# Optimization experiments

Measured on AMD Instinct MI355X. Metric: run time of the kernel, lower is better.

## Reference

```python
import jax, jax.numpy as jnp
import numpy as np

KH = KW = 3
STRIDE = 1
PAD = 1
DIL = 1


def _bilinear_sample(x, py, px):
    """Zero-padded bilinear sampling.
    x: [B, C, H, W]; py, px: [B, K2, Ho, Wo] float sample coords.
    returns [B, C, K2, Ho, Wo].
    """
    B, C, H, W = x.shape
    y0 = jnp.floor(py)
    x0 = jnp.floor(px)
    wy1 = py - y0
    wx1 = px - x0
    wy0 = 1.0 - wy1
    wx0 = 1.0 - wx1
    xf = x.reshape(B, C, H * W)

    def gather(iy, ix):
        valid = (iy >= 0) & (iy <= H - 1) & (ix >= 0) & (ix <= W - 1)
        iyc = jnp.clip(iy, 0, H - 1).astype(jnp.int32)
        ixc = jnp.clip(ix, 0, W - 1).astype(jnp.int32)
        idx = (iyc * W + ixc).reshape(B, 1, -1)  # [B,1,K2*Ho*Wo]
        v = jnp.take_along_axis(xf, idx, axis=2)
        v = v.reshape(B, C, *iy.shape[1:])
        return v * valid[:, None].astype(x.dtype)

    return (gather(y0, x0) * (wy0 * wx0)[:, None]
            + gather(y0, x0 + 1) * (wy0 * wx1)[:, None]
            + gather(y0 + 1, x0) * (wy1 * wx0)[:, None]
            + gather(y0 + 1, x0 + 1) * (wy1 * wx1)[:, None])


def setup_inputs() -> dict:
    key = jax.random.key(0)
    k1, k2, k3, k4 = jax.random.split(key, 4)
    B, C, H, W = 8, 64, 128, 128
    Cout = 64
    K2 = KH * KW
    x = jax.random.normal(k1, (B, C, H, W), dtype=jnp.float32)
    offset = jax.random.normal(k2, (B, 2 * K2, H, W), dtype=jnp.float32)
    mask = jax.random.uniform(k3, (B, K2, H, W), dtype=jnp.float32)
    n = C * KH * KW
    stdv = 1.0 / np.sqrt(n)
    weight = jax.random.uniform(k4, (Cout, C, KH, KW), dtype=jnp.float32,
                                minval=-stdv, maxval=stdv)
    bias = jnp.zeros((Cout,), dtype=jnp.float32)
    return {"x": x, "offset": offset, "mask": mask, "weight": weight, "bias": bias}


def reference(x, offset, mask, weight, bias):
    B, C, H, W = x.shape
    Cout, Cin, kh, kw = weight.shape
    K2 = kh * kw
    Ho = (H + 2 * PAD - (DIL * (kh - 1) + 1)) // STRIDE + 1
    Wo = (W + 2 * PAD - (DIL * (kw - 1) + 1)) // STRIDE + 1
    # offset channels come interleaved per kernel location: ::2 -> x, 1::2 -> y
    off = offset.reshape(B, K2, 2, Ho, Wo)
    dx = off[:, :, 0]  # [B,K2,Ho,Wo]
    dy = off[:, :, 1]
    base_y = (STRIDE * jnp.arange(Ho) - PAD).astype(x.dtype)  # [Ho]
    base_x = (STRIDE * jnp.arange(Wo) - PAD).astype(x.dtype)  # [Wo]
    ky = (DIL * jnp.arange(kh)).astype(x.dtype)
    kx = (DIL * jnp.arange(kw)).astype(x.dtype)
    koff_y = jnp.repeat(ky, kw)  # [K2]
    koff_x = jnp.tile(kx, kh)    # [K2]
    py = base_y[None, None, :, None] + koff_y[None, :, None, None] + dy
    px = base_x[None, None, None, :] + koff_x[None, :, None, None] + dx
    sampled = _bilinear_sample(x, py, px)          # [B,C,K2,Ho,Wo]
    sampled = sampled * mask[:, None]              # modulation
    w = weight.reshape(Cout, Cin * K2)
    cols = sampled.reshape(B, Cin * K2, Ho, Wo)
    out = jnp.einsum('bqhw,oq->bohw', cols, w) + bias[None, :, None, None]
    return out
```

## Files before the change

### kernel.cpp

```cpp
#include <hip/hip_runtime.h>
#include <hip/hip_bf16.h>


constexpr int B    = 8;
constexpr int C    = 64;
constexpr int H    = 128;
constexpr int W    = 128;
constexpr int COUT = 64;
constexpr int K2   = 9;
constexpr int HW   = H * W;
constexpr int TPX  = 64;

typedef __attribute__((ext_vector_type(8))) short bf16x8;
typedef __attribute__((ext_vector_type(4))) float f32x4;
typedef __attribute__((ext_vector_type(2))) float f32x2;

constexpr int LDSS = 72;

#define LDS_BARRIER() asm volatile("s_waitcnt lgkmcnt(0)\n\ts_barrier" ::: "memory")

__global__ __launch_bounds__(256) void transpose_x_kernel(
    const float* __restrict__ x, short* __restrict__ xt) {
    __shared__ float tbuf[64][65];
    const int blk  = blockIdx.x;
    const int b    = blk >> 8;
    const int hwb  = (blk & 255) * 64;
    const int lane = threadIdx.x & 63;
    const int grp  = threadIdx.x >> 6;
    const float* xb = x + (size_t)b * C * HW;
#pragma unroll
    for (int r = 0; r < 16; ++r) {
        const int c = grp * 16 + r;
        tbuf[c][lane] = xb[c * HW + hwb + lane];
    }
    __syncthreads();
    short* xo = xt + (size_t)b * HW * C;
#pragma unroll
    for (int r = 0; r < 16; ++r) {
        const int hw_l = grp * 16 + r;
        union { __hip_bfloat16 h; short s; } u;
        u.h = __float2bfloat16(tbuf[lane][hw_l]);
        xo[(size_t)(hwb + hw_l) * C + lane] = u.s;
    }
}

__global__ __launch_bounds__(256) void pack_w_kernel(
    const float* __restrict__ w, short* __restrict__ wfrag) {
    int id = blockIdx.x * blockDim.x + threadIdx.x;
    if (id >= COUT * C * K2) return;
    const int j    = id & 7;
    const int lane = (id >> 3) & 63;
    const int mt   = (id >> 9) & 3;
    const int kk   = (id >> 11) & 1;
    const int k    = id >> 12;
    const int m    = mt * 16 + (lane & 15);
    const int q    = lane >> 4;
    const int c    = kk * 32 + q * 8 + j;
    union { __hip_bfloat16 h; short s; } u;
    u.h = __float2bfloat16(w[(m * C + c) * K2 + k]);
    wfrag[id] = u.s;
}

__global__ __launch_bounds__(512, 4) void mdcn_pc_kernel(
    const short* __restrict__ xt,
    const float* __restrict__ offset,
    const float* __restrict__ mask,
    const short* __restrict__ wfrag,
    const float* __restrict__ bias,
    float* __restrict__ out) {

    __shared__ short smem[2][TPX * LDSS];
    __shared__ int4   pidx[K2 * TPX];
    __shared__ float4 pwts[K2 * TPX];

    const int wg   = blockIdx.x;
    const int b    = wg & 7;
    const int t    = wg >> 3;
    const int ho   = t >> 1;
    const int px0  = (t & 1) * TPX;

    const int tid  = threadIdx.x;
    const int wave = tid >> 6;

    for (int f = tid; f < K2 * TPX; f += 512) {
        const int k = f >> 6;
        const int i = f & 63;
        const int wo = px0 + i;
        const int ky = k / 3, kx = k % 3;
        const float dx = offset[(((size_t)b * 2 * K2 + 2 * k    ) * H + ho) * W + wo];
        const float dy = offset[(((size_t)b * 2 * K2 + 2 * k + 1) * H + ho) * W + wo];
        const float mm = mask  [(((size_t)b * K2     + k        ) * H + ho) * W + wo];
        const float py = (float)(ho - 1 + ky) + dy;
        const float px = (float)(wo - 1 + kx) + dx;
        const float y0f = floorf(py), x0f = floorf(px);
        const float wy1 = py - y0f,   wx1 = px - x0f;
        const float wy0 = 1.0f - wy1, wx0 = 1.0f - wx1;
        const int iy0 = (int)y0f, ix0 = (int)x0f;
        const int iy1 = iy0 + 1,  ix1 = ix0 + 1;
        const bool vy0 = (iy0 >= 0) & (iy0 < H);
        const bool vy1 = (iy1 >= 0) & (iy1 < H);
        const bool vx0 = (ix0 >= 0) & (ix0 < W);
        const bool vx1 = (ix1 >= 0) & (ix1 < W);
        float4 wv;
        wv.x = (vy0 & vx0) ? wy0 * wx0 * mm : 0.0f;
        wv.y = (vy0 & vx1) ? wy0 * wx1 * mm : 0.0f;
        wv.z = (vy1 & vx0) ? wy1 * wx0 * mm : 0.0f;
        wv.w = (vy1 & vx1) ? wy1 * wx1 * mm : 0.0f;
        const int cy0 = min(max(iy0, 0), H - 1);
        const int cy1 = min(max(iy1, 0), H - 1);
        const int cx0 = min(max(ix0, 0), W - 1);
        const int cx1 = min(max(ix1, 0), W - 1);
        int4 bv;
        bv.x = (cy0 * W + cx0) * (C * 2);
        bv.y = (cy0 * W + cx1) * (C * 2);
        bv.z = (cy1 * W + cx0) * (C * 2);
        bv.w = (cy1 * W + cx1) * (C * 2);
        pidx[f] = bv;
        pwts[f] = wv;
    }
    __syncthreads();

    if (wave < 4) {
        const int spx = tid >> 2;
        const int cq  = (tid & 3) * 16;
        const char* xb =
            (const char*)(xt + (size_t)b * HW * C) + cq * 2;

        for (int k = 0; k < K2; ++k) {
            const int4   bi = pidx[k * 64 + spx];
            const float4 wv = pwts[k * 64 + spx];
            const short* s00 = (const short*)(xb + bi.x);
            const short* s01 = (const short*)(xb + bi.y);
            const short* s10 = (const short*)(xb + bi.z);
            const short* s11 = (const short*)(xb + bi.w);

            short* dst = &smem[k & 1][spx * LDSS + cq];
#pragma unroll
            for (int h = 0; h < 2; ++h) {
                const bf16x8 g00 = *(const bf16x8*)(s00 + h * 8);
                const bf16x8 g01 = *(const bf16x8*)(s01 + h * 8);
                const bf16x8 g10 = *(const bf16x8*)(s10 + h * 8);
                const bf16x8 g11 = *(const bf16x8*)(s11 + h * 8);
                union U8 { bf16x8 s; __hip_bfloat162 h2[4]; };
                U8 u00{g00}, u01{g01}, u10{g10}, u11{g11}, rr;
#pragma unroll
                for (int p = 0; p < 4; ++p) {
                    const float2 a00 = __bfloat1622float2(u00.h2[p]);
                    const float2 a01 = __bfloat1622float2(u01.h2[p]);
                    const float2 a10 = __bfloat1622float2(u10.h2[p]);
                    const float2 a11 = __bfloat1622float2(u11.h2[p]);
                    f32x2 f00 = {a00.x, a00.y}, f01 = {a01.x, a01.y};
                    f32x2 f10 = {a10.x, a10.y}, f11 = {a11.x, a11.y};
                    f32x2 v = f00 * wv.x + f01 * wv.y + f10 * wv.z + f11 * wv.w;
                    rr.h2[p] = __float22bfloat162_rn(float2{v.x, v.y});
                }
                *(bf16x8*)(dst + h * 8) = rr.s;
            }
            LDS_BARRIER();
        }
    } else {
        const int widx = wave - 4;
        const int lane = tid & 63;
        const int col  = lane & 15;
        const int q    = lane >> 4;
        const int pix  = widx * 16 + col;
        const bf16x8* wf = (const bf16x8*)wfrag;

        f32x4 acc[4];
#pragma unroll
        for (int mt = 0; mt < 4; ++mt) acc[mt] = (f32x4)0.0f;

        for (int k = 0; k < K2; ++k) {
            LDS_BARRIER();
            bf16x8 af[8];
#pragma unroll
            for (int i = 0; i < 8; ++i) af[i] = wf[(k * 8 + i) * 64 + lane];
#pragma unroll
            for (int kk = 0; kk < 2; ++kk) {
                const bf16x8 bfrag =
                    *(const bf16x8*)(&smem[k & 1][pix * LDSS + kk * 32 + q * 8]);
#pragma unroll
                for (int mt = 0; mt < 4; ++mt)
                    acc[mt] = __builtin_amdgcn_mfma_f32_16x16x32_bf16(
                        af[kk * 4 + mt], bfrag, acc[mt], 0, 0, 0);
            }
        }

        const int wo = px0 + pix;
#pragma unroll
        for (int mt = 0; mt < 4; ++mt) {
#pragma unroll
            for (int r = 0; r < 4; ++r) {
                const int o = mt * 16 + q * 4 + r;
                out[(((size_t)b * COUT + o) * H + ho) * W + wo] =
                    acc[mt][r] + bias[o];
            }
        }
    }
}

__global__ __launch_bounds__(256) void mdcn_direct_kernel(
    const float* __restrict__ x, const float* __restrict__ offset,
    const float* __restrict__ mask, const float* __restrict__ wsrc,
    const float* __restrict__ bias, float* __restrict__ out) {
    const int p  = blockIdx.x * blockDim.x + threadIdx.x;
    const int wo = p & (W - 1);
    const int ho = (p >> 7) & (H - 1);
    const int b  = p >> 14;
    float acc[COUT];
#pragma unroll
    for (int o = 0; o < COUT; ++o) acc[o] = bias[o];
    const float* xb = x + b * C * HW;
    for (int k = 0; k < K2; ++k) {
        const int ky = k / 3, kx = k % 3;
        const float dx = offset[((b * 2 * K2 + 2 * k    ) * H + ho) * W + wo];
        const float dy = offset[((b * 2 * K2 + 2 * k + 1) * H + ho) * W + wo];
        const float m  = mask  [((b * K2     + k        ) * H + ho) * W + wo];
        const float py = (float)(ho - 1 + ky) + dy;
        const float px = (float)(wo - 1 + kx) + dx;
        const float y0f = floorf(py), x0f = floorf(px);
        const float wy1 = py - y0f, wx1 = px - x0f;
        const float wy0 = 1.0f - wy1, wx0 = 1.0f - wx1;
        const int iy0 = (int)y0f, ix0 = (int)x0f;
        const int iy1 = iy0 + 1, ix1 = ix0 + 1;
        const bool vy0 = (iy0 >= 0) & (iy0 < H);
        const bool vy1 = (iy1 >= 0) & (iy1 < H);
        const bool vx0 = (ix0 >= 0) & (ix0 < W);
        const bool vx1 = (ix1 >= 0) & (ix1 < W);
        const float w00 = (vy0 & vx0) ? wy0 * wx0 * m : 0.0f;
        const float w01 = (vy0 & vx1) ? wy0 * wx1 * m : 0.0f;
        const float w10 = (vy1 & vx0) ? wy1 * wx0 * m : 0.0f;
        const float w11 = (vy1 & vx1) ? wy1 * wx1 * m : 0.0f;
        const int cy0 = min(max(iy0, 0), H - 1);
        const int cy1 = min(max(iy1, 0), H - 1);
        const int cx0 = min(max(ix0, 0), W - 1);
        const int cx1 = min(max(ix1, 0), W - 1);
        const int o00 = cy0 * W + cx0, o01 = cy0 * W + cx1;
        const int o10 = cy1 * W + cx0, o11 = cy1 * W + cx1;
        for (int c = 0; c < C; ++c) {
            const float* xp = xb + c * HW;
            const float val = w00 * xp[o00] + w01 * xp[o01] +
                              w10 * xp[o10] + w11 * xp[o11];
#pragma unroll
            for (int o = 0; o < COUT; ++o)
                acc[o] += wsrc[(o * C + c) * K2 + k] * val;
        }
    }
    float* op = out + ((size_t)b * COUT) * HW + ho * W + wo;
#pragma unroll
    for (int o = 0; o < COUT; ++o) op[o * HW] = acc[o];
}

extern "C" void kernel_launch(void* const* d_in, const int* in_sizes, int n_in,
                              void* d_out, int out_size, void* d_ws, size_t ws_size,
                              hipStream_t stream) {
    const float* x      = (const float*)d_in[0];
    const float* offset = (const float*)d_in[1];
    const float* mask   = (const float*)d_in[2];
    const float* weight = (const float*)d_in[3];
    const float* bias   = (const float*)d_in[4];
    float* out          = (float*)d_out;

    const size_t xt_bytes = (size_t)B * HW * C * sizeof(short);
    const size_t wf_bytes = (size_t)COUT * C * K2 * sizeof(short);
    if (ws_size >= xt_bytes + wf_bytes) {
        short* xt    = (short*)d_ws;
        short* wfrag = (short*)((char*)d_ws + xt_bytes);
        transpose_x_kernel<<<B * (HW / 64), 256, 0, stream>>>(x, xt);
        pack_w_kernel<<<(COUT * C * K2 + 255) / 256, 256, 0, stream>>>(weight, wfrag);
        mdcn_pc_kernel<<<2 * B * H, 512, 0, stream>>>(xt, offset, mask, wfrag, bias, out);
    } else {
        mdcn_direct_kernel<<<(B * HW) / 256, 256, 0, stream>>>(
            x, offset, mask, weight, bias, out);
    }
}
```

Baseline: 142.5 us.

## Fuse bilinear gather into MFMA waves, removing producer/consumer LDS staging

Replaces the warp-specialized design, where four waves gathered and interpolated samples into double-buffered LDS and four other waves ran MFMA, with a single set of four waves. Each wave gathers its own B-fragment directly in MFMA lane layout and feeds it straight into the matrix instructions. Per-tap barriers and LDS staging go away, and the next tap's indices and weights are prefetched. The trade-off is that each thread now does both the gather and the compute, with block size halved and higher per-thread register pressure.

```diff
diff --git a/kernel.cpp b/kernel.cpp
--- a/kernel.cpp
+++ b/kernel.cpp
@@ -14,10 +14,6 @@
 typedef __attribute__((ext_vector_type(8))) short bf16x8;
 typedef __attribute__((ext_vector_type(4))) float f32x4;
 typedef __attribute__((ext_vector_type(2))) float f32x2;
-
-constexpr int LDSS = 72;
-
-#define LDS_BARRIER() asm volatile("s_waitcnt lgkmcnt(0)\n\ts_barrier" ::: "memory")
 
 __global__ __launch_bounds__(256) void transpose_x_kernel(
     const float* __restrict__ x, short* __restrict__ xt) {
@@ -61,7 +57,7 @@
     wfrag[id] = u.s;
 }
 
-__global__ __launch_bounds__(512, 4) void mdcn_pc_kernel(
+__global__ __launch_bounds__(256, 4) void mdcn_fused_kernel(
     const short* __restrict__ xt,
     const float* __restrict__ offset,
     const float* __restrict__ mask,
@@ -69,7 +65,6 @@
     const float* __restrict__ bias,
     float* __restrict__ out) {
 
-    __shared__ short smem[2][TPX * LDSS];
     __shared__ int4   pidx[K2 * TPX];
     __shared__ float4 pwts[K2 * TPX];
 
@@ -78,11 +73,9 @@
     const int t    = wg >> 3;
     const int ho   = t >> 1;
     const int px0  = (t & 1) * TPX;
-
     const int tid  = threadIdx.x;
-    const int wave = tid >> 6;
-
-    for (int f = tid; f < K2 * TPX; f += 512) {
+
+    for (int f = tid; f < K2 * TPX; f += 256) {
         const int k = f >> 6;
         const int i = f & 63;
         const int wo = px0 + i;
@@ -120,81 +113,92 @@
     }
     __syncthreads();
 
-    if (wave < 4) {
-        const int spx = tid >> 2;
-        const int cq  = (tid & 3) * 16;
-        const char* xb =
-            (const char*)(xt + (size_t)b * HW * C) + cq * 2;
-
-        for (int k = 0; k < K2; ++k) {
-            const int4   bi = pidx[k * 64 + spx];
-            const float4 wv = pwts[k * 64 + spx];
-            const short* s00 = (const short*)(xb + bi.x);
-            const short* s01 = (const short*)(xb + bi.y);
-            const short* s10 = (const short*)(xb + bi.z);
-            const short* s11 = (const short*)(xb + bi.w);
-
-            short* dst = &smem[k & 1][spx * LDSS + cq];
-#pragma unroll
-            for (int h = 0; h < 2; ++h) {
-                const bf16x8 g00 = *(const bf16x8*)(s00 + h * 8);
-                const bf16x8 g01 = *(const bf16x8*)(s01 + h * 8);
-                const bf16x8 g10 = *(const bf16x8*)(s10 + h * 8);
-                const bf16x8 g11 = *(const bf16x8*)(s11 + h * 8);
-                union U8 { bf16x8 s; __hip_bfloat162 h2[4]; };
-                U8 u00{g00}, u01{g01}, u10{g10}, u11{g11}, rr;
-#pragma unroll
-                for (int p = 0; p < 4; ++p) {
-                    const float2 a00 = __bfloat1622float2(u00.h2[p]);
-                    const float2 a01 = __bfloat1622float2(u01.h2[p]);
-                    const float2 a10 = __bfloat1622float2(u10.h2[p]);
-                    const float2 a11 = __bfloat1622float2(u11.h2[p]);
-                    f32x2 f00 = {a00.x, a00.y}, f01 = {a01.x, a01.y};
-                    f32x2 f10 = {a10.x, a10.y}, f11 = {a11.x, a11.y};
-                    f32x2 v = f00 * wv.x + f01 * wv.y + f10 * wv.z + f11 * wv.w;
-                    rr.h2[p] = __float22bfloat162_rn(float2{v.x, v.y});
-                }
-                *(bf16x8*)(dst + h * 8) = rr.s;
+    const int lane = tid & 63;
+    const int wave = tid >> 6;
+    const int col  = lane & 15;
+    const int q    = lane >> 4;
+    const int pl   = wave * 16 + col;
+    const int wo   = px0 + pl;
+
+    const char* xb = (const char*)(xt + (size_t)b * HW * C) + q * 16;
+    const bf16x8* wf = (const bf16x8*)wfrag;
+
+    f32x4 acc[4];
+#pragma unroll
+    for (int mt = 0; mt < 4; ++mt) acc[mt] = (f32x4)0.0f;
+
+    int4   bi = pidx[pl];
+    float4 wv = pwts[pl];
+
+#pragma unroll 1
+    for (int k = 0; k < K2; ++k) {
+        const char* s00 = xb + bi.x;
+        const char* s01 = xb + bi.y;
+        const char* s10 = xb + bi.z;
+        const char* s11 = xb + bi.w;
+        const bf16x8 g00a = *(const bf16x8*)(s00);
+        const bf16x8 g01a = *(const bf16x8*)(s01);
+        const bf16x8 g10a = *(const bf16x8*)(s10);
+        const bf16x8 g11a = *(const bf16x8*)(s11);
+        const bf16x8 g00b = *(const bf16x8*)(s00 + 64);
+        const bf16x8 g01b = *(const bf16x8*)(s01 + 64);
+        const bf16x8 g10b = *(const bf16x8*)(s10 + 64);
+        const bf16x8 g11b = *(const bf16x8*)(s11 + 64);
+
+        bf16x8 af[8];
+#pragma unroll
+        for (int i = 0; i < 8; ++i) af[i] = wf[(k * 8 + i) * 64 + lane];
+
+        const int kn = (k < K2 - 1) ? (k + 1) : k;
+        const int4   nbi = pidx[kn * 64 + pl];
+        const float4 nwv = pwts[kn * 64 + pl];
+
+        union U8 { bf16x8 s; __hip_bfloat162 h2[4]; };
+        {
+            U8 u00{g00a}, u01{g01a}, u10{g10a}, u11{g11a}, rr;
+#pragma unroll
+            for (int p = 0; p < 4; ++p) {
+                const float2 a00 = __bfloat1622float2(u00.h2[p]);
+                const float2 a01 = __bfloat1622float2(u01.h2[p]);
+                const float2 a10 = __bfloat1622float2(u10.h2[p]);
+                const float2 a11 = __bfloat1622float2(u11.h2[p]);
+                f32x2 v = f32x2{a00.x, a00.y} * wv.x + f32x2{a01.x, a01.y} * wv.y
+                        + f32x2{a10.x, a10.y} * wv.z + f32x2{a11.x, a11.y} * wv.w;
+                rr.h2[p] = __float22bfloat162_rn(float2{v.x, v.y});
             }
-            LDS_BARRIER();
-        }
-    } else {
-        const int widx = wave - 4;
-        const int lane = tid & 63;
-        const int col  = lane & 15;
-        const int q    = lane >> 4;
-        const int pix  = widx * 16 + col;
-        const bf16x8* wf = (const bf16x8*)wfrag;
-
-        f32x4 acc[4];
-#pragma unroll
-        for (int mt = 0; mt < 4; ++mt) acc[mt] = (f32x4)0.0f;
-
-        for (int k = 0; k < K2; ++k) {
-            LDS_BARRIER();
-            bf16x8 af[8];
-#pragma unroll
-            for (int i = 0; i < 8; ++i) af[i] = wf[(k * 8 + i) * 64 + lane];
-#pragma unroll
-            for (int kk = 0; kk < 2; ++kk) {
-                const bf16x8 bfrag =
-                    *(const bf16x8*)(&smem[k & 1][pix * LDSS + kk * 32 + q * 8]);
-#pragma unroll
-                for (int mt = 0; mt < 4; ++mt)
-                    acc[mt] = __builtin_amdgcn_mfma_f32_16x16x32_bf16(
-                        af[kk * 4 + mt], bfrag, acc[mt], 0, 0, 0);
+#pragma unroll
+            for (int mt = 0; mt < 4; ++mt)
+                acc[mt] = __builtin_amdgcn_mfma_f32_16x16x32_bf16(
+                    af[mt], rr.s, acc[mt], 0, 0, 0);
+        }
+        {
+            U8 u00{g00b}, u01{g01b}, u10{g10b}, u11{g11b}, rr;
+#pragma unroll
+            for (int p = 0; p < 4; ++p) {
+                const float2 a00 = __bfloat1622float2(u00.h2[p]);
+                const float2 a01 = __bfloat1622float2(u01.h2[p]);
+                const float2 a10 = __bfloat1622float2(u10.h2[p]);
+                const float2 a11 = __bfloat1622float2(u11.h2[p]);
+                f32x2 v = f32x2{a00.x, a00.y} * wv.x + f32x2{a01.x, a01.y} * wv.y
+                        + f32x2{a10.x, a10.y} * wv.z + f32x2{a11.x, a11.y} * wv.w;
+                rr.h2[p] = __float22bfloat162_rn(float2{v.x, v.y});
             }
-        }
-
-        const int wo = px0 + pix;
-#pragma unroll
-        for (int mt = 0; mt < 4; ++mt) {
-#pragma unroll
-            for (int r = 0; r < 4; ++r) {
-                const int o = mt * 16 + q * 4 + r;
-                out[(((size_t)b * COUT + o) * H + ho) * W + wo] =
-                    acc[mt][r] + bias[o];
-            }
+#pragma unroll
+            for (int mt = 0; mt < 4; ++mt)
+                acc[mt] = __builtin_amdgcn_mfma_f32_16x16x32_bf16(
+                    af[4 + mt], rr.s, acc[mt], 0, 0, 0);
+        }
+        bi = nbi;
+        wv = nwv;
+    }
+
+#pragma unroll
+    for (int mt = 0; mt < 4; ++mt) {
+#pragma unroll
+        for (int r = 0; r < 4; ++r) {
+            const int o = mt * 16 + q * 4 + r;
+            out[(((size_t)b * COUT + o) * H + ho) * W + wo] =
+                acc[mt][r] + bias[o];
         }
     }
 }
@@ -268,7 +272,7 @@
         short* wfrag = (short*)((char*)d_ws + xt_bytes);
         transpose_x_kernel<<<B * (HW / 64), 256, 0, stream>>>(x, xt);
         pack_w_kernel<<<(COUT * C * K2 + 255) / 256, 256, 0, stream>>>(weight, wfrag);
-        mdcn_pc_kernel<<<2 * B * H, 512, 0, stream>>>(xt, offset, mask, wfrag, bias, out);
+        mdcn_fused_kernel<<<2 * B * H, 256, 0, stream>>>(xt, offset, mask, wfrag, bias, out);
     } else {
         mdcn_direct_kernel<<<(B * HW) / 256, 256, 0, stream>>>(
             x, offset, mask, weight, bias, out);
```

Result: slower. 181.8 us (+27.6%).
